# Kernel tuning notes

Hardware: AMD Instinct MI355X
Metric: run time of the kernel (lower is better)

Reference implementation:

```python
import jax, jax.numpy as jnp
import numpy as np

Z_RES, N_RES = 128, 512
M_PTS = 2_000_000


def trilinear_devoxelize(grid, coords):
    """Gather-based trilinear interpolation.
    grid:   (Z, N, N, C) voxel grid
    coords: (M, 3) float positions in voxel index space (z, x, y)
    returns (M, C)
    """
    Zd, Nd = grid.shape[0], grid.shape[1]
    c0f = jnp.floor(coords)
    frac = coords - c0f                      # (M, 3) fractional offsets
    maxi = jnp.array([Zd - 1, Nd - 1, Nd - 1], dtype=jnp.int32)
    c0 = jnp.clip(c0f.astype(jnp.int32), 0, maxi)
    c1 = jnp.clip(c0 + 1, 0, maxi)
    fz, fx, fy = frac[:, 0:1], frac[:, 1:2], frac[:, 2:3]
    gz, gx, gy = 1.0 - fz, 1.0 - fx, 1.0 - fy

    def g(zi, xi, yi):
        return grid[zi, xi, yi]              # (M, C) gather

    out = (g(c0[:, 0], c0[:, 1], c0[:, 2]) * gz * gx * gy
         + g(c0[:, 0], c0[:, 1], c1[:, 2]) * gz * gx * fy
         + g(c0[:, 0], c1[:, 1], c0[:, 2]) * gz * fx * gy
         + g(c0[:, 0], c1[:, 1], c1[:, 2]) * gz * fx * fy
         + g(c1[:, 0], c0[:, 1], c0[:, 2]) * fz * gx * gy
         + g(c1[:, 0], c0[:, 1], c1[:, 2]) * fz * gx * fy
         + g(c1[:, 0], c1[:, 1], c0[:, 2]) * fz * fx * gy
         + g(c1[:, 0], c1[:, 1], c1[:, 2]) * fz * fx * fy)
    return out


def setup_inputs() -> dict:
    key = jax.random.key(0)
    k1, k2 = jax.random.split(key)
    extents = jnp.array([Z_RES - 1, N_RES - 1, N_RES - 1], jnp.float32)
    coords = jax.random.uniform(k1, (M_PTS, 3), dtype=jnp.float32) * extents
    # init_scale = 1.0 -> albedo ~ U[0,1); normal initialized to zeros (per module)
    albedo = jax.random.uniform(k2, (Z_RES, N_RES, N_RES), dtype=jnp.float32)
    normal = jnp.zeros((Z_RES, N_RES, N_RES, 3), dtype=jnp.float32)
    return {"coords": coords, "albedo": albedo, "normal": normal}


def reference(coords, albedo, normal):
    base_normal = jnp.array([-1.0, 0.0, 0.0], dtype=jnp.float32)
    a = trilinear_devoxelize(albedo[..., None], coords)[:, 0]   # (M,)
    n = trilinear_devoxelize(normal, coords)                    # (M, 3)
    a = jax.nn.elu(a)
    n = jnp.tanh(n) + base_normal
    # F.normalize(dim=1, eps=1e-12): divide by max(||n||, eps)
    norm = jnp.maximum(jnp.linalg.norm(n, axis=1, keepdims=True), 1e-12)
    n = n / norm
    return (a, n)
```

## Files before the change

kernel.cpp:

```cpp
#include <hip/hip_runtime.h>
#include <math.h>

#define ZR 128
#define NR 512

typedef unsigned int u32x4 __attribute__((ext_vector_type(4)));
typedef unsigned short u16x8 __attribute__((ext_vector_type(8)));


__device__ __forceinline__ float bf16_to_f32(unsigned short u) {
    return __uint_as_float(((unsigned int)u) << 16);
}

__device__ __forceinline__ unsigned short f32_to_bf16_rne(float v) {
    unsigned int u = __float_as_uint(v);
    return (unsigned short)((u + 0x7FFFu + ((u >> 16) & 1u)) >> 16);
}

__device__ __forceinline__ void zcheck_range(
    const u32x4* __restrict__ normal4, long long lo, long long hi,
    long long rank, long long nthreads, unsigned int* __restrict__ flag)
{
    unsigned int acc = 0;
    for (long long i = lo + rank * 256 + threadIdx.x; i < hi; i += nthreads) {
        u32x4 v = __builtin_nontemporal_load(&normal4[i]);
        acc |= v.x | v.y | v.z | v.w;
    }
    if (__ballot(acc != 0) && ((threadIdx.x & 63) == 0))
        atomicOr(flag, 1u);
}

__global__ __launch_bounds__(256) void repack_zcheck_kernel(
    const float* __restrict__ albedo,
    unsigned short* __restrict__ tiled,
    const u32x4* __restrict__ normal4,
    unsigned int* __restrict__ flag,
    long long n4h)
{
    unsigned int b = blockIdx.x;
    if (b < 4096u) {
        zcheck_range(normal4, 0, n4h, (long long)b, 4096LL * 256, flag);
        return;
    }
    unsigned int b2 = b - 4096u;
    int z = (int)(b2 >> 7);
    int xt = (int)(b2 & 127u);

    __shared__ float s[2048];
    const float* src = albedo + ((size_t)z * NR + (size_t)xt * 4) * NR;
    for (int k = threadIdx.x; k < 512; k += 256)
        ((float4*)s)[k] = ((const float4*)src)[k];
    __syncthreads();

    unsigned short* dst = tiled + (size_t)b2 * 2048;
    int t8 = threadIdx.x * 8;
    u16x8 outv;
#pragma unroll
    for (int j = 0; j < 8; j++) {
        int k = t8 + j;
        int yt = k >> 5;
        int r = k & 31;
        int xr = r >> 3;
        int yy = r & 7;
        outv[j] = f32_to_bf16_rne(s[xr * 512 + (yt << 3) + yy]);
    }
    *(u16x8*)(dst + t8) = outv;
}

#define K2_ZBLK 1536
__global__ __launch_bounds__(256) void interp_zcheck_kernel(
    const float* __restrict__ coords,
    const unsigned short* __restrict__ tiled,
    const u32x4* __restrict__ normal4,
    const unsigned int* __restrict__ normal_tail,
    int tail_cnt,
    unsigned int* __restrict__ flag,
    float* __restrict__ out_a,
    float* __restrict__ out_n,
    int M, long long n4h, long long n4)
{
    unsigned int b = blockIdx.x;
    if (b < K2_ZBLK) {
        if (b == 0 && threadIdx.x < (unsigned)tail_cnt) {
            unsigned int tv = normal_tail[threadIdx.x];
            if (tv) atomicOr(flag, 1u);
        }
        zcheck_range(normal4, n4h, n4, (long long)b, (long long)K2_ZBLK * 256, flag);
        return;
    }
    int i = (int)(b - K2_ZBLK) * 256 + threadIdx.x;
    if (i >= M) return;

    float cz = coords[3 * i + 0];
    float cx = coords[3 * i + 1];
    float cy = coords[3 * i + 2];

    float fz0 = floorf(cz), fx0 = floorf(cx), fy0 = floorf(cy);
    float fz = cz - fz0, fx = cx - fx0, fy = cy - fy0;

    int z0 = min(max((int)fz0, 0), ZR - 1);
    int x0 = min(max((int)fx0, 0), NR - 1);
    int y0 = min(max((int)fy0, 0), NR - 1);
    int z1 = min(z0 + 1, ZR - 1);
    int x1 = min(x0 + 1, NR - 1);
    int y1 = min(y0 + 1, NR - 1);

    float gz = 1.0f - fz, gx = 1.0f - fx, gy = 1.0f - fy;

    float w000 = gz * gx * gy, w001 = gz * gx * fy;
    float w010 = gz * fx * gy, w011 = gz * fx * fy;
    float w100 = fz * gx * gy, w101 = fz * gx * fy;
    float w110 = fz * fx * gy, w111 = fz * fx * fy;

    int xo0 = (x0 & 3) << 3, xo1 = (x1 & 3) << 3;
    int yo0 = y0 & 7,        yo1 = y1 & 7;
    int c0 = (y0 >> 3) << 5, c1 = (y1 >> 3) << 5;
    int r00 = ((z0 << 7) + (x0 >> 2)) << 11;
    int r01 = ((z0 << 7) + (x1 >> 2)) << 11;
    int r10 = ((z1 << 7) + (x0 >> 2)) << 11;
    int r11 = ((z1 << 7) + (x1 >> 2)) << 11;

    float a =
        bf16_to_f32(tiled[r00 + c0 + xo0 + yo0]) * w000 +
        bf16_to_f32(tiled[r00 + c1 + xo0 + yo1]) * w001 +
        bf16_to_f32(tiled[r01 + c0 + xo1 + yo0]) * w010 +
        bf16_to_f32(tiled[r01 + c1 + xo1 + yo1]) * w011 +
        bf16_to_f32(tiled[r10 + c0 + xo0 + yo0]) * w100 +
        bf16_to_f32(tiled[r10 + c1 + xo0 + yo1]) * w101 +
        bf16_to_f32(tiled[r11 + c0 + xo1 + yo0]) * w110 +
        bf16_to_f32(tiled[r11 + c1 + xo1 + yo1]) * w111;

    a = (a > 0.0f) ? a : expm1f(a);

    out_a[i] = a;
    out_n[3 * i + 0] = -1.0f;
    out_n[3 * i + 1] = 0.0f;
    out_n[3 * i + 2] = 0.0f;
}

__global__ __launch_bounds__(256) void normal_full_kernel(
    const float* __restrict__ coords,
    const float* __restrict__ normal,
    const unsigned int* __restrict__ flag,
    float* __restrict__ out_n,
    int M)
{
    if (*flag == 0) return;

    int stride = gridDim.x * 256;
    for (int i = blockIdx.x * 256 + threadIdx.x; i < M; i += stride) {
        float cz = coords[3 * i + 0];
        float cx = coords[3 * i + 1];
        float cy = coords[3 * i + 2];

        float fz0 = floorf(cz), fx0 = floorf(cx), fy0 = floorf(cy);
        float fz = cz - fz0, fx = cx - fx0, fy = cy - fy0;

        int z0 = min(max((int)fz0, 0), ZR - 1);
        int x0 = min(max((int)fx0, 0), NR - 1);
        int y0 = min(max((int)fy0, 0), NR - 1);
        int z1 = min(z0 + 1, ZR - 1);
        int x1 = min(x0 + 1, NR - 1);
        int y1 = min(y0 + 1, NR - 1);

        float gz = 1.0f - fz, gx = 1.0f - fx, gy = 1.0f - fy;

        float w000 = gz * gx * gy, w001 = gz * gx * fy;
        float w010 = gz * fx * gy, w011 = gz * fx * fy;
        float w100 = fz * gx * gy, w101 = fz * gx * fy;
        float w110 = fz * fx * gy, w111 = fz * fx * fy;

        size_t b00 = ((size_t)z0 * NR + x0) * NR;
        size_t b01 = ((size_t)z0 * NR + x1) * NR;
        size_t b10 = ((size_t)z1 * NR + x0) * NR;
        size_t b11 = ((size_t)z1 * NR + x1) * NR;

        float n0 = 0.0f, n1 = 0.0f, n2 = 0.0f;
#define ACC(base, yy, w)                                           \
        {                                                          \
            const float* q = normal + ((base) + (size_t)(yy)) * 3; \
            n0 += q[0] * (w);                                      \
            n1 += q[1] * (w);                                      \
            n2 += q[2] * (w);                                      \
        }
        ACC(b00, y0, w000); ACC(b00, y1, w001);
        ACC(b01, y0, w010); ACC(b01, y1, w011);
        ACC(b10, y0, w100); ACC(b10, y1, w101);
        ACC(b11, y0, w110); ACC(b11, y1, w111);
#undef ACC

        n0 = tanhf(n0) - 1.0f;
        n1 = tanhf(n1);
        n2 = tanhf(n2);

        float nrm = sqrtf(n0 * n0 + n1 * n1 + n2 * n2);
        nrm = fmaxf(nrm, 1e-12f);
        float inv = 1.0f / nrm;

        out_n[3 * i + 0] = n0 * inv;
        out_n[3 * i + 1] = n1 * inv;
        out_n[3 * i + 2] = n2 * inv;
    }
}

__global__ __launch_bounds__(256) void devox_direct(
    const float* __restrict__ coords,
    const float* __restrict__ albedo,
    const float* __restrict__ normal,
    float* __restrict__ out_a,
    float* __restrict__ out_n,
    int M)
{
    int i = blockIdx.x * 256 + threadIdx.x;
    if (i >= M) return;

    float cz = coords[3 * i + 0];
    float cx = coords[3 * i + 1];
    float cy = coords[3 * i + 2];

    float fz0 = floorf(cz), fx0 = floorf(cx), fy0 = floorf(cy);
    float fz = cz - fz0, fx = cx - fx0, fy = cy - fy0;

    int z0 = min(max((int)fz0, 0), ZR - 1);
    int x0 = min(max((int)fx0, 0), NR - 1);
    int y0 = min(max((int)fy0, 0), NR - 1);
    int z1 = min(z0 + 1, ZR - 1);
    int x1 = min(x0 + 1, NR - 1);
    int y1 = min(y0 + 1, NR - 1);

    float gz = 1.0f - fz, gx = 1.0f - fx, gy = 1.0f - fy;
    float w000 = gz * gx * gy, w001 = gz * gx * fy;
    float w010 = gz * fx * gy, w011 = gz * fx * fy;
    float w100 = fz * gx * gy, w101 = fz * gx * fy;
    float w110 = fz * fx * gy, w111 = fz * fx * fy;

    size_t b00 = ((size_t)z0 * NR + x0) * NR;
    size_t b01 = ((size_t)z0 * NR + x1) * NR;
    size_t b10 = ((size_t)z1 * NR + x0) * NR;
    size_t b11 = ((size_t)z1 * NR + x1) * NR;

    float a =
        albedo[b00 + y0] * w000 + albedo[b00 + y1] * w001 +
        albedo[b01 + y0] * w010 + albedo[b01 + y1] * w011 +
        albedo[b10 + y0] * w100 + albedo[b10 + y1] * w101 +
        albedo[b11 + y0] * w110 + albedo[b11 + y1] * w111;

    float n0 = 0.0f, n1 = 0.0f, n2 = 0.0f;
#define ACC(base, yy, w)                                           \
    {                                                              \
        const float* q = normal + ((base) + (size_t)(yy)) * 3;     \
        n0 += q[0] * (w);                                          \
        n1 += q[1] * (w);                                          \
        n2 += q[2] * (w);                                          \
    }
    ACC(b00, y0, w000); ACC(b00, y1, w001);
    ACC(b01, y0, w010); ACC(b01, y1, w011);
    ACC(b10, y0, w100); ACC(b10, y1, w101);
    ACC(b11, y0, w110); ACC(b11, y1, w111);
#undef ACC

    a = (a > 0.0f) ? a : expm1f(a);
    n0 = tanhf(n0) - 1.0f;
    n1 = tanhf(n1);
    n2 = tanhf(n2);
    float nrm = sqrtf(n0 * n0 + n1 * n1 + n2 * n2);
    nrm = fmaxf(nrm, 1e-12f);
    float inv = 1.0f / nrm;

    out_a[i] = a;
    out_n[3 * i + 0] = n0 * inv;
    out_n[3 * i + 1] = n1 * inv;
    out_n[3 * i + 2] = n2 * inv;
}

extern "C" void kernel_launch(void* const* d_in, const int* in_sizes, int n_in,
                              void* d_out, int out_size, void* d_ws, size_t ws_size,
                              hipStream_t stream) {
    const float* coords = (const float*)d_in[0];
    const float* albedo = (const float*)d_in[1];
    const float* normal = (const float*)d_in[2];

    int M = in_sizes[0] / 3;
    long long normal_elems = (long long)in_sizes[2];
    long long n4 = normal_elems / 4;
    long long n4h = n4 / 2;
    int tail_cnt = (int)(normal_elems & 3);
    const unsigned int* normal_tail = (const unsigned int*)normal + n4 * 4;

    float* out = (float*)d_out;
    float* out_a = out;
    float* out_n = out + M;

    size_t tiled_off = 256;
    size_t tiled_bytes = (size_t)128 * 128 * 64 * 32 * 2;
    if (ws_size < tiled_off + tiled_bytes) {
        int nblk = (M + 255) / 256;
        devox_direct<<<nblk, 256, 0, stream>>>(coords, albedo, normal, out_a, out_n, M);
        return;
    }

    unsigned int* flag = (unsigned int*)d_ws;
    unsigned short* tiled = (unsigned short*)((char*)d_ws + tiled_off);

    hipMemsetAsync(flag, 0, sizeof(unsigned int), stream);

    repack_zcheck_kernel<<<4096 + 16384, 256, 0, stream>>>(
        albedo, tiled, (const u32x4*)normal, flag, n4h);

    int iblk = (M + 255) / 256;
    interp_zcheck_kernel<<<K2_ZBLK + iblk, 256, 0, stream>>>(
        coords, tiled, (const u32x4*)normal, normal_tail, tail_cnt,
        flag, out_a, out_n, M, n4h, n4);

    normal_full_kernel<<<2048, 256, 0, stream>>>(coords, normal, flag, out_n, M);
}
```

Baseline: 667.9 us.

## Bucket points by z-slab via histogram scatter before albedo interpolation

Adds a histogram pass over z-indices and a scatter kernel that writes points, with their original indices, into z-sorted records. Interpolation then walks these records, so consecutive threads touch the same albedo slabs and gathers hit cache better. The constant normal output fill is vectorised with float4 stores, the zero check on the normal grid is unrolled by two, and the albedo repack now uses nontemporal loads. In exchange it adds an extra coords pass, a 16-byte record per point of workspace traffic, and scattered writes to out_a.

```diff
diff --git a/kernel.cpp b/kernel.cpp
--- a/kernel.cpp
+++ b/kernel.cpp
@@ -3,6 +3,7 @@
 
 #define ZR 128
 #define NR 512
+#define SC_PTS 2048
 
 typedef unsigned int u32x4 __attribute__((ext_vector_type(4)));
 typedef unsigned short u16x8 __attribute__((ext_vector_type(8)));
@@ -22,7 +23,13 @@
     long long rank, long long nthreads, unsigned int* __restrict__ flag)
 {
     unsigned int acc = 0;
-    for (long long i = lo + rank * 256 + threadIdx.x; i < hi; i += nthreads) {
+    long long i = lo + rank * 256 + threadIdx.x;
+    for (; i + nthreads < hi; i += 2 * nthreads) {
+        u32x4 v0 = __builtin_nontemporal_load(&normal4[i]);
+        u32x4 v1 = __builtin_nontemporal_load(&normal4[i + nthreads]);
+        acc |= v0.x | v0.y | v0.z | v0.w | v1.x | v1.y | v1.z | v1.w;
+    }
+    if (i < hi) {
         u32x4 v = __builtin_nontemporal_load(&normal4[i]);
         acc |= v.x | v.y | v.z | v.w;
     }
@@ -30,26 +37,82 @@
         atomicOr(flag, 1u);
 }
 
-__global__ __launch_bounds__(256) void repack_zcheck_kernel(
+__device__ __forceinline__ float interp_one(
+    const unsigned short* __restrict__ tiled,
+    float cz, float cx, float cy)
+{
+    float fz0 = floorf(cz), fx0 = floorf(cx), fy0 = floorf(cy);
+    float fz = cz - fz0, fx = cx - fx0, fy = cy - fy0;
+
+    int z0 = min(max((int)fz0, 0), ZR - 1);
+    int x0 = min(max((int)fx0, 0), NR - 1);
+    int y0 = min(max((int)fy0, 0), NR - 1);
+    int z1 = min(z0 + 1, ZR - 1);
+    int x1 = min(x0 + 1, NR - 1);
+    int y1 = min(y0 + 1, NR - 1);
+
+    float gz = 1.0f - fz, gx = 1.0f - fx, gy = 1.0f - fy;
+
+    float w000 = gz * gx * gy, w001 = gz * gx * fy;
+    float w010 = gz * fx * gy, w011 = gz * fx * fy;
+    float w100 = fz * gx * gy, w101 = fz * gx * fy;
+    float w110 = fz * fx * gy, w111 = fz * fx * fy;
+
+    int xo0 = (x0 & 3) << 3, xo1 = (x1 & 3) << 3;
+    int yo0 = y0 & 7,        yo1 = y1 & 7;
+    int c0 = (y0 >> 3) << 5, c1 = (y1 >> 3) << 5;
+    int r00 = ((z0 << 7) + (x0 >> 2)) << 11;
+    int r01 = ((z0 << 7) + (x1 >> 2)) << 11;
+    int r10 = ((z1 << 7) + (x0 >> 2)) << 11;
+    int r11 = ((z1 << 7) + (x1 >> 2)) << 11;
+
+    return
+        bf16_to_f32(tiled[r00 + c0 + xo0 + yo0]) * w000 +
+        bf16_to_f32(tiled[r00 + c1 + xo0 + yo1]) * w001 +
+        bf16_to_f32(tiled[r01 + c0 + xo1 + yo0]) * w010 +
+        bf16_to_f32(tiled[r01 + c1 + xo1 + yo1]) * w011 +
+        bf16_to_f32(tiled[r10 + c0 + xo0 + yo0]) * w100 +
+        bf16_to_f32(tiled[r10 + c1 + xo0 + yo1]) * w101 +
+        bf16_to_f32(tiled[r11 + c0 + xo1 + yo0]) * w110 +
+        bf16_to_f32(tiled[r11 + c1 + xo1 + yo1]) * w111;
+}
+
+__global__ __launch_bounds__(256) void repack_hist_kernel(
     const float* __restrict__ albedo,
+    const float* __restrict__ coords,
     unsigned short* __restrict__ tiled,
-    const u32x4* __restrict__ normal4,
-    unsigned int* __restrict__ flag,
-    long long n4h)
-{
+    unsigned int* __restrict__ g_hist,
+    int M)
+{
+    __shared__ float s[2048];
     unsigned int b = blockIdx.x;
-    if (b < 4096u) {
-        zcheck_range(normal4, 0, n4h, (long long)b, 4096LL * 256, flag);
+
+    if (b < 1024u) {
+        unsigned int* lh = (unsigned int*)s;
+        if (threadIdx.x < 128) lh[threadIdx.x] = 0;
+        __syncthreads();
+        for (int i = (int)b * 256 + threadIdx.x; i < M; i += 1024 * 256) {
+            float cz = coords[3 * (size_t)i];
+            int bk = min(max((int)floorf(cz), 0), ZR - 1);
+            atomicAdd(&lh[bk], 1u);
+        }
+        __syncthreads();
+        if (threadIdx.x < 128) {
+            unsigned int c = lh[threadIdx.x];
+            if (c) atomicAdd(&g_hist[threadIdx.x * 16], c);
+        }
         return;
     }
-    unsigned int b2 = b - 4096u;
+
+    unsigned int b2 = b - 1024u;
     int z = (int)(b2 >> 7);
     int xt = (int)(b2 & 127u);
 
-    __shared__ float s[2048];
-    const float* src = albedo + ((size_t)z * NR + (size_t)xt * 4) * NR;
-    for (int k = threadIdx.x; k < 512; k += 256)
-        ((float4*)s)[k] = ((const float4*)src)[k];
+    const u32x4* src = (const u32x4*)(albedo + ((size_t)z * NR + (size_t)xt * 4) * NR);
+    for (int k = threadIdx.x; k < 512; k += 256) {
+        u32x4 v = __builtin_nontemporal_load(&src[k]);
+        ((u32x4*)s)[k] = v;
+    }
     __syncthreads();
 
     unsigned short* dst = tiled + (size_t)b2 * 2048;
@@ -67,75 +130,140 @@
     *(u16x8*)(dst + t8) = outv;
 }
 
-#define K2_ZBLK 1536
-__global__ __launch_bounds__(256) void interp_zcheck_kernel(
+__global__ __launch_bounds__(256) void scatter_kernel(
     const float* __restrict__ coords,
+    const unsigned int* __restrict__ g_hist,
+    unsigned int* __restrict__ g_cursor,
+    float4* __restrict__ rec,
+    int M)
+{
+    __shared__ unsigned int cnt[128];
+    __shared__ unsigned int sc[128];
+    __shared__ unsigned int bs[128];
+
+    int tid = threadIdx.x;
+    int start = (int)blockIdx.x * SC_PTS;
+
+    float cz[8], cx[8], cy[8];
+    int bk[8];
+#pragma unroll
+    for (int k = 0; k < 8; k++) {
+        int i = start + k * 256 + tid;
+        if (i < M) {
+            size_t o = 3 * (size_t)i;
+            cz[k] = coords[o];
+            cx[k] = coords[o + 1];
+            cy[k] = coords[o + 2];
+            bk[k] = min(max((int)floorf(cz[k]), 0), ZR - 1);
+        } else {
+            bk[k] = -1;
+        }
+    }
+
+    if (tid < 128) cnt[tid] = 0;
+    __syncthreads();
+#pragma unroll
+    for (int k = 0; k < 8; k++)
+        if (bk[k] >= 0) atomicAdd(&cnt[bk[k]], 1u);
+    __syncthreads();
+
+    unsigned int hv = 0, myofs = 0;
+    if (tid < 128) {
+        unsigned int c = cnt[tid];
+        if (c) myofs = atomicAdd(&g_cursor[tid * 16], c);
+        hv = g_hist[tid * 16];
+        sc[tid] = hv;
+    }
+    __syncthreads();
+    for (int off = 1; off < 128; off <<= 1) {
+        unsigned int v = 0;
+        if (tid < 128 && tid >= off) v = sc[tid - off];
+        __syncthreads();
+        if (tid < 128) sc[tid] += v;
+        __syncthreads();
+    }
+    if (tid < 128) {
+        bs[tid] = (sc[tid] - hv) + myofs;
+        cnt[tid] = 0;
+    }
+    __syncthreads();
+
+#pragma unroll
+    for (int k = 0; k < 8; k++) {
+        if (bk[k] >= 0) {
+            unsigned int lr = atomicAdd(&cnt[bk[k]], 1u);
+            unsigned int pos = bs[bk[k]] + lr;
+            int i = start + k * 256 + tid;
+            float4 r;
+            r.x = cz[k]; r.y = cx[k]; r.z = cy[k];
+            r.w = __uint_as_float((unsigned int)i);
+            rec[pos] = r;
+        }
+    }
+}
+
+__global__ __launch_bounds__(256) void interp_fill_zcheck_kernel(
+    const float4* __restrict__ rec,
     const unsigned short* __restrict__ tiled,
     const u32x4* __restrict__ normal4,
-    const unsigned int* __restrict__ normal_tail,
-    int tail_cnt,
+    const unsigned int* __restrict__ normal_tail, int tail_cnt,
     unsigned int* __restrict__ flag,
     float* __restrict__ out_a,
     float* __restrict__ out_n,
-    int M, long long n4h, long long n4)
+    int M, long long n4, int IB, int FB)
 {
     unsigned int b = blockIdx.x;
-    if (b < K2_ZBLK) {
-        if (b == 0 && threadIdx.x < (unsigned)tail_cnt) {
-            unsigned int tv = normal_tail[threadIdx.x];
-            if (tv) atomicOr(flag, 1u);
-        }
-        zcheck_range(normal4, n4h, n4, (long long)b, (long long)K2_ZBLK * 256, flag);
+
+    if (b < (unsigned)IB) {
+        unsigned int q = (unsigned)IB >> 3, r = (unsigned)IB & 7;
+        unsigned int x = b & 7, sgrp = b >> 3;
+        unsigned int sb = (x < r ? x * (q + 1) : r * (q + 1) + (x - r) * q) + sgrp;
+
+        int t = (int)sb * 256 + (int)threadIdx.x;
+        int p0 = t * 2;
+        if (p0 >= M) return;
+
+        float4 r0 = rec[p0];
+        float a0 = interp_one(tiled, r0.x, r0.y, r0.z);
+        a0 = (a0 > 0.0f) ? a0 : expm1f(a0);
+        out_a[__float_as_uint(r0.w)] = a0;
+
+        if (p0 + 1 < M) {
+            float4 r1 = rec[p0 + 1];
+            float a1 = interp_one(tiled, r1.x, r1.y, r1.z);
+            a1 = (a1 > 0.0f) ? a1 : expm1f(a1);
+            out_a[__float_as_uint(r1.w)] = a1;
+        }
         return;
     }
-    int i = (int)(b - K2_ZBLK) * 256 + threadIdx.x;
-    if (i >= M) return;
-
-    float cz = coords[3 * i + 0];
-    float cx = coords[3 * i + 1];
-    float cy = coords[3 * i + 2];
-
-    float fz0 = floorf(cz), fx0 = floorf(cx), fy0 = floorf(cy);
-    float fz = cz - fz0, fx = cx - fx0, fy = cy - fy0;
-
-    int z0 = min(max((int)fz0, 0), ZR - 1);
-    int x0 = min(max((int)fx0, 0), NR - 1);
-    int y0 = min(max((int)fy0, 0), NR - 1);
-    int z1 = min(z0 + 1, ZR - 1);
-    int x1 = min(x0 + 1, NR - 1);
-    int y1 = min(y0 + 1, NR - 1);
-
-    float gz = 1.0f - fz, gx = 1.0f - fx, gy = 1.0f - fy;
-
-    float w000 = gz * gx * gy, w001 = gz * gx * fy;
-    float w010 = gz * fx * gy, w011 = gz * fx * fy;
-    float w100 = fz * gx * gy, w101 = fz * gx * fy;
-    float w110 = fz * fx * gy, w111 = fz * fx * fy;
-
-    int xo0 = (x0 & 3) << 3, xo1 = (x1 & 3) << 3;
-    int yo0 = y0 & 7,        yo1 = y1 & 7;
-    int c0 = (y0 >> 3) << 5, c1 = (y1 >> 3) << 5;
-    int r00 = ((z0 << 7) + (x0 >> 2)) << 11;
-    int r01 = ((z0 << 7) + (x1 >> 2)) << 11;
-    int r10 = ((z1 << 7) + (x0 >> 2)) << 11;
-    int r11 = ((z1 << 7) + (x1 >> 2)) << 11;
-
-    float a =
-        bf16_to_f32(tiled[r00 + c0 + xo0 + yo0]) * w000 +
-        bf16_to_f32(tiled[r00 + c1 + xo0 + yo1]) * w001 +
-        bf16_to_f32(tiled[r01 + c0 + xo1 + yo0]) * w010 +
-        bf16_to_f32(tiled[r01 + c1 + xo1 + yo1]) * w011 +
-        bf16_to_f32(tiled[r10 + c0 + xo0 + yo0]) * w100 +
-        bf16_to_f32(tiled[r10 + c1 + xo0 + yo1]) * w101 +
-        bf16_to_f32(tiled[r11 + c0 + xo1 + yo0]) * w110 +
-        bf16_to_f32(tiled[r11 + c1 + xo1 + yo1]) * w111;
-
-    a = (a > 0.0f) ? a : expm1f(a);
-
-    out_a[i] = a;
-    out_n[3 * i + 0] = -1.0f;
-    out_n[3 * i + 1] = 0.0f;
-    out_n[3 * i + 2] = 0.0f;
+
+    if (b < (unsigned)(IB + FB)) {
+        unsigned int fidx = b - (unsigned)IB;
+        long long total = 3LL * M;
+        if ((M & 3) == 0) {
+            long long f4 = (long long)fidx * 256 + threadIdx.x;
+            long long nf4 = total >> 2;
+            if (f4 < nf4) {
+                int rmod = (int)(f4 % 3);
+                float4 v;
+                if (rmod == 0)      { v.x = -1.f; v.y =  0.f; v.z =  0.f; v.w = -1.f; }
+                else if (rmod == 1) { v.x =  0.f; v.y =  0.f; v.z = -1.f; v.w =  0.f; }
+                else                { v.x =  0.f; v.y = -1.f; v.z =  0.f; v.w =  0.f; }
+                ((float4*)out_n)[f4] = v;
+            }
+        } else {
+            long long stride = (long long)FB * 256;
+            for (long long qq = (long long)fidx * 256 + threadIdx.x; qq < total; qq += stride)
+                out_n[qq] = ((qq % 3) == 0) ? -1.0f : 0.0f;
+        }
+        return;
+    }
+
+    unsigned int zidx = b - (unsigned)(IB + FB);
+    if (zidx == 0 && threadIdx.x < (unsigned)tail_cnt) {
+        if (normal_tail[threadIdx.x]) atomicOr(flag, 1u);
+    }
+    zcheck_range(normal4, 0, n4, (long long)zidx, 1024LL * 256, flag);
 }
 
 __global__ __launch_bounds__(256) void normal_full_kernel(
@@ -178,10 +306,10 @@
         float n0 = 0.0f, n1 = 0.0f, n2 = 0.0f;
 #define ACC(base, yy, w)                                           \
         {                                                          \
-            const float* q = normal + ((base) + (size_t)(yy)) * 3; \
-            n0 += q[0] * (w);                                      \
-            n1 += q[1] * (w);                                      \
-            n2 += q[2] * (w);                                      \
+            const float* qp = normal + ((base) + (size_t)(yy)) * 3;\
+            n0 += qp[0] * (w);                                     \
+            n1 += qp[1] * (w);                                     \
+            n2 += qp[2] * (w);                                     \
         }
         ACC(b00, y0, w000); ACC(b00, y1, w001);
         ACC(b01, y0, w010); ACC(b01, y1, w011);
@@ -248,10 +376,10 @@
     float n0 = 0.0f, n1 = 0.0f, n2 = 0.0f;
 #define ACC(base, yy, w)                                           \
     {                                                              \
-        const float* q = normal + ((base) + (size_t)(yy)) * 3;     \
-        n0 += q[0] * (w);                                          \
-        n1 += q[1] * (w);                                          \
-        n2 += q[2] * (w);                                          \
+        const float* qp = normal + ((base) + (size_t)(yy)) * 3;    \
+        n0 += qp[0] * (w);                                         \
+        n1 += qp[1] * (w);                                         \
+        n2 += qp[2] * (w);                                         \
     }
     ACC(b00, y0, w000); ACC(b00, y1, w001);
     ACC(b01, y0, w010); ACC(b01, y1, w011);
@@ -283,7 +411,6 @@
     int M = in_sizes[0] / 3;
     long long normal_elems = (long long)in_sizes[2];
     long long n4 = normal_elems / 4;
-    long long n4h = n4 / 2;
     int tail_cnt = (int)(normal_elems & 3);
     const unsigned int* normal_tail = (const unsigned int*)normal + n4 * 4;
 
@@ -291,8 +418,10 @@
     float* out_a = out;
     float* out_n = out + M;
 
-    size_t tiled_off = 256;
-    size_t tiled_bytes = (size_t)128 * 128 * 64 * 32 * 2;
+    size_t rec_off = 32768;
+    size_t rec_bytes = (size_t)M * 16;
+    size_t tiled_off = rec_off + rec_bytes;
+    size_t tiled_bytes = (size_t)ZR * NR * NR * 2;
     if (ws_size < tiled_off + tiled_bytes) {
         int nblk = (M + 255) / 256;
         devox_direct<<<nblk, 256, 0, stream>>>(coords, albedo, normal, out_a, out_n, M);
@@ -300,17 +429,28 @@
     }
 
     unsigned int* flag = (unsigned int*)d_ws;
+    unsigned int* g_hist = (unsigned int*)((char*)d_ws + 4096);
+    unsigned int* g_cursor = (unsigned int*)((char*)d_ws + 12288);
+    float4* rec = (float4*)((char*)d_ws + rec_off);
     unsigned short* tiled = (unsigned short*)((char*)d_ws + tiled_off);
 
-    hipMemsetAsync(flag, 0, sizeof(unsigned int), stream);
-
-    repack_zcheck_kernel<<<4096 + 16384, 256, 0, stream>>>(
-        albedo, tiled, (const u32x4*)normal, flag, n4h);
-
-    int iblk = (M + 255) / 256;
-    interp_zcheck_kernel<<<K2_ZBLK + iblk, 256, 0, stream>>>(
-        coords, tiled, (const u32x4*)normal, normal_tail, tail_cnt,
-        flag, out_a, out_n, M, n4h, n4);
+    (void)hipMemsetAsync(d_ws, 0, 20480, stream);
+
+    repack_hist_kernel<<<1024 + 16384, 256, 0, stream>>>(albedo, coords, tiled, g_hist, M);
+
+    int CB = (M + SC_PTS - 1) / SC_PTS;
+    if (CB < 1) CB = 1;
+    scatter_kernel<<<CB, 256, 0, stream>>>(coords, g_hist, g_cursor, rec, M);
+
+    int IB = (M + 511) / 512;
+    if (IB < 1) IB = 1;
+    long long total_n = 3LL * M;
+    int FB = ((M & 3) == 0) ? (int)((total_n / 4 + 255) / 256) : 2048;
+    if (FB < 1) FB = 1;
+    int G = IB + FB + 1024;
+    interp_fill_zcheck_kernel<<<G, 256, 0, stream>>>(
+        rec, tiled, (const u32x4*)normal, normal_tail, tail_cnt,
+        flag, out_a, out_n, M, n4, IB, FB);
 
     normal_full_kernel<<<2048, 256, 0, stream>>>(coords, normal, flag, out_n, M);
 }
```

Result: slower. 719.4 us (+7.7%).
